# Performance work log

Measured on AMD Instinct MI355X. Metric: run time of the kernel, lower is better.

## Reference

```python
import jax, jax.numpy as jnp
import numpy as np

FEAT = 256
BS = 64
L = 2048
TAU = 2.0          # maxTemp * tempDecay**0 with numUpdates=0
MIN_SEG = 3.0      # minSegmentWidth
NEG_BIG = -10000.0


def setup_inputs() -> dict:
    key = jax.random.key(0)
    ks = jax.random.split(key, 8)
    s = 1.0 / np.sqrt(FEAT)  # PyTorch LSTM/Linear uniform init bound
    x = jax.random.normal(ks[0], (BS, L, FEAT), jnp.float32)
    label = jax.random.randint(ks[1], (BS, L), 0, 2)
    # LSTM cell params (PyTorch layout: gates ordered i, f, g, o)
    W_ih = jax.random.uniform(ks[2], (4 * FEAT, FEAT + 1), jnp.float32, -s, s)
    W_hh = jax.random.uniform(ks[3], (4 * FEAT, FEAT), jnp.float32, -s, s)
    b_ih = jax.random.uniform(ks[4], (4 * FEAT,), jnp.float32, -s, s)
    b_hh = jax.random.uniform(ks[5], (4 * FEAT,), jnp.float32, -s, s)
    # policy: Linear(featuresDim, 2)
    Wp = jax.random.uniform(ks[6], (2, FEAT), jnp.float32, -s, s)
    bp = jax.random.uniform(ks[7], (2,), jnp.float32, -s, s)
    return {"x": x, "label": label, "W_ih": W_ih, "W_hh": W_hh,
            "b_ih": b_ih, "b_hh": b_hh, "Wp": Wp, "bp": bp}


def reference(x, label, W_ih, W_hh, b_ih, b_hh, Wp, bp):
    # label is accepted by the original forward but never used.
    bs, l, d = x.shape

    def step(carry, xt):
        prev_b, flag, h, c = carry  # prev boundary [bs], noBoundaryFlag [bs], LSTM state [bs,d]
        inp = jnp.concatenate([prev_b[:, None], xt], axis=-1)  # [bs, d+1]
        gates = inp @ W_ih.T + h @ W_hh.T + b_ih + b_hh        # [bs, 4d]
        i, f, g, o = jnp.split(gates, 4, axis=-1)
        c = jax.nn.sigmoid(f) * c + jax.nn.sigmoid(i) * jnp.tanh(g)
        h = jax.nn.sigmoid(o) * jnp.tanh(c)
        logits = h @ Wp.T + bp                                 # [bs, 2]
        # mask boundary logit where a boundary was emitted within minSegmentWidth
        logits = logits.at[:, 1].add(jnp.where(flag > 0, NEG_BIG, 0.0))
        logp = jax.nn.log_softmax(logits / TAU, axis=-1)
        samp = jnp.argmax(logp, axis=-1)                       # eval-mode sampling
        flag = jnp.where(flag > 0, flag - 1.0, flag)
        flag = jnp.where(samp > 0, MIN_SEG, flag)
        return (samp.astype(x.dtype), flag, h, c), (logp, samp)

    init = (jnp.zeros((bs,), x.dtype), jnp.zeros((bs,), x.dtype),
            jnp.zeros((bs, d), x.dtype), jnp.zeros((bs, d), x.dtype))
    _, (logps, samps) = jax.lax.scan(step, init, jnp.swapaxes(x, 0, 1))
    logps = jnp.swapaxes(logps, 0, 1)                  # [bs, l, 2]
    boundaries = jnp.swapaxes(samps, 0, 1).astype(x.dtype)  # [bs, l]
    sel = jnp.take_along_axis(logps, boundaries[..., None].astype(jnp.int32), axis=-1)  # [bs, l, 1]
    return boundaries, sel
```

## Files before the change

kernel.cpp:

```cpp
#include <hip/hip_runtime.h>
#include <cstdint>
#include <cmath>

#define FEAT 256
#define GATES 1024
#define BS 64
#define SEQ 2048
#define NEG_BIG -10000.0f
#define MIN_SEG 3.0f

#define KK_REG 24
#define KK_LDS 8
#define KK_STA (KK_REG + KK_LDS)
#define NGEMM 192

#define M0_WPB  262144
#define M0_BIAS 263168
#define M0_H    264192
#define M0_C    280576
#define M0_PF   296960
#define M0_XP   297984
#define M1_WIT  262144
#define M1_WPB  524288
#define M1_BIAS 525312

template<int MODE>
__global__ __launch_bounds__(1024) void prep_kernel(
    const float* __restrict__ W_ih, const float* __restrict__ W_hh,
    const float* __restrict__ b_ih, const float* __restrict__ b_hh,
    float* __restrict__ ws)
{
    const int k = blockIdx.x;
    const int j = threadIdx.x;
    ws[k * GATES + j] = W_hh[(size_t)j * FEAT + k];
    if (MODE == 1)
        ws[M1_WIT + k * GATES + j] = W_ih[(size_t)j * (FEAT + 1) + 1 + k];
    if (k == 0) {
        const int WPB = MODE ? M1_WPB : M0_WPB;
        const int BIA = MODE ? M1_BIAS : M0_BIAS;
        ws[WPB + j] = W_ih[(size_t)j * (FEAT + 1)];
        ws[BIA + j] = b_ih[j] + b_hh[j];
    }
    if (MODE == 0 && k == 1) {
#pragma unroll
        for (int i = 0; i < 16; ++i) {
            ws[M0_H + i * 1024 + j] = 0.f;
            ws[M0_C + i * 1024 + j] = 0.f;
        }
        if (j < 128) ws[M0_PF + j] = 0.f;
    }
}

__global__ __launch_bounds__(256) void xproj_gemm(
    const float* __restrict__ x, const float* __restrict__ W_ih,
    float* __restrict__ ws, int t0, int xpoff)
{
    const int trow = blockIdx.y;
    const int t  = t0 + trow;
    const int j0 = blockIdx.x * 64;
    const int tid = threadIdx.x;
    const int ty = tid >> 4, tx = tid & 15;
    const float* bias = ws + M0_BIAS;
    float* XP = ws + xpoff;
    __shared__ __align__(16) float As[64][65];
    __shared__ __align__(16) float Bs[64][65];
    float acc[4][4] = {};
    for (int k0 = 0; k0 < FEAT; k0 += 64) {
#pragma unroll
        for (int i = 0; i < 16; ++i) {
            int idx = i * 256 + tid;
            int rr = idx >> 6, cc = idx & 63;
            As[rr][cc] = x[((size_t)rr * SEQ + t) * FEAT + k0 + cc];
        }
#pragma unroll
        for (int i = 0; i < 16; ++i) {
            int idx = i * 256 + tid;
            int jj = idx >> 6, kk = idx & 63;
            Bs[kk][jj] = W_ih[(size_t)(j0 + jj) * (FEAT + 1) + 1 + k0 + kk];
        }
        __syncthreads();
#pragma unroll
        for (int kk = 0; kk < 64; ++kk) {
            float a[4], bv[4];
#pragma unroll
            for (int r = 0; r < 4; ++r) a[r] = As[ty * 4 + r][kk];
#pragma unroll
            for (int c = 0; c < 4; ++c) bv[c] = Bs[kk][tx * 4 + c];
#pragma unroll
            for (int r = 0; r < 4; ++r)
#pragma unroll
                for (int c = 0; c < 4; ++c)
                    acc[r][c] = fmaf(a[r], bv[c], acc[r][c]);
        }
        __syncthreads();
    }
#pragma unroll
    for (int r = 0; r < 4; ++r) {
        int bb = ty * 4 + r;
        size_t base = ((size_t)trow * BS + bb) * GATES + j0 + tx * 4;
        float4 v;
        v.x = acc[r][0] + bias[j0 + tx * 4 + 0];
        v.y = acc[r][1] + bias[j0 + tx * 4 + 1];
        v.z = acc[r][2] + bias[j0 + tx * 4 + 2];
        v.w = acc[r][3] + bias[j0 + tx * 4 + 3];
        *(float4*)&XP[base] = v;
    }
}

#define FMA4(acc, hb, wv) \
    acc.x = fmaf(hb, wv.x, acc.x); acc.y = fmaf(hb, wv.y, acc.y); \
    acc.z = fmaf(hb, wv.z, acc.z); acc.w = fmaf(hb, wv.w, acc.w);

__global__ __launch_bounds__(1024, 1) void fused_kernel(
    const float* __restrict__ x, const float* __restrict__ W_ih,
    float* __restrict__ ws,
    const float* __restrict__ Wp, const float* __restrict__ bp,
    float* __restrict__ out_b, float* __restrict__ out_sel,
    int t0, int Tlen, int xp_cur, int xp_nxt)
{
    __shared__ __align__(16) float smem[39178];
    const int tid = threadIdx.x;

    if (blockIdx.x >= BS) {
        if (xp_nxt < 0) return;
        float* As = smem;
        float* Bs = smem + 4160;
        const float* bias = ws + M0_BIAS;
        float* XPn = ws + xp_nxt;
        const int ty = tid >> 6, tx = tid & 63;
        const int jobs = Tlen * 4;
        for (int job = blockIdx.x - BS; job < jobs; job += NGEMM) {
            const int trow = job >> 2;
            const int j0 = (job & 3) * 256;
            const int t = t0 + Tlen + trow;
            float acc[4][4] = {};
            for (int k0 = 0; k0 < FEAT; k0 += 64) {
                __syncthreads();
#pragma unroll
                for (int i = 0; i < 4; ++i) {
                    int idx = i * 1024 + tid, rr = idx >> 6, cc = idx & 63;
                    As[rr * 65 + cc] = x[((size_t)rr * SEQ + t) * FEAT + k0 + cc];
                }
#pragma unroll
                for (int i = 0; i < 16; ++i) {
                    int idx = i * 1024 + tid, jj = idx >> 6, kk = idx & 63;
                    Bs[kk * 260 + jj] = W_ih[(size_t)(j0 + jj) * (FEAT + 1) + 1 + k0 + kk];
                }
                __syncthreads();
#pragma unroll
                for (int kk = 0; kk < 64; ++kk) {
                    float4 bv = *(const float4*)&Bs[kk * 260 + tx * 4];
                    float a[4];
#pragma unroll
                    for (int r = 0; r < 4; ++r) a[r] = As[(ty * 4 + r) * 65 + kk];
#pragma unroll
                    for (int r = 0; r < 4; ++r) {
                        acc[r][0] = fmaf(a[r], bv.x, acc[r][0]);
                        acc[r][1] = fmaf(a[r], bv.y, acc[r][1]);
                        acc[r][2] = fmaf(a[r], bv.z, acc[r][2]);
                        acc[r][3] = fmaf(a[r], bv.w, acc[r][3]);
                    }
                }
            }
#pragma unroll
            for (int r = 0; r < 4; ++r) {
                int bb = ty * 4 + r;
                size_t base = ((size_t)trow * BS + bb) * GATES + j0 + tx * 4;
                float4 v;
                v.x = acc[r][0] + bias[j0 + tx * 4 + 0];
                v.y = acc[r][1] + bias[j0 + tx * 4 + 1];
                v.z = acc[r][2] + bias[j0 + tx * 4 + 2];
                v.w = acc[r][3] + bias[j0 + tx * 4 + 3];
                *(float4*)&XPn[base] = v;
            }
        }
        return;
    }

    const int b   = blockIdx.x;
    const int ch  = tid >> 8;
    const int j4  = (tid & 255) * 4;
    const int f   = tid & 255;
    const int kbase = ch * 64;

    const float* WT   = ws;
    const float* WPB  = ws + M0_WPB;
    float* H  = ws + M0_H;
    float* C  = ws + M0_C;
    float* PF = ws + M0_PF;
    const float* XPc = ws + xp_cur;

    float* wlds   = smem;
    float* part   = smem + 32768;
    float* h_lds  = smem + 36864;
    float* xp_lds = smem + 37120;
    float* red    = smem + 39168;
    float* s_pv   = smem + 39176;

    float4 wreg[KK_REG];
#pragma unroll
    for (int kk = 0; kk < KK_REG; ++kk)
        wreg[kk] = *(const float4*)&WT[(size_t)(kbase + kk) * GATES + j4];
#pragma unroll
    for (int i = 0; i < 4 * KK_LDS; ++i) {
        int ch2 = i / KK_LDS, kkl = i % KK_LDS;
        wlds[i * 1024 + tid] = WT[(size_t)(ch2 * 64 + KK_REG + kkl) * GATES + tid];
    }

    float wpbr[4] = {};
    float wp0 = 0.f, wp1 = 0.f, c_reg = 0.f;
    if (tid < FEAT) {
#pragma unroll
        for (int g = 0; g < 4; ++g) wpbr[g] = WPB[g * FEAT + f];
        wp0 = Wp[f]; wp1 = Wp[FEAT + f];
        c_reg = C[b * FEAT + f];
        h_lds[f] = H[b * FEAT + f];
    }
    const float bp0 = bp[0], bp1 = bp[1];
    xp_lds[tid] = XPc[(size_t)b * GATES + tid];
    if (tid == 0) { s_pv[0] = PF[b * 2 + 0]; s_pv[1] = PF[b * 2 + 1]; }
    __syncthreads();

    float fl_r = 0.f;
    if (tid == 0) fl_r = s_pv[1];

    for (int tl = 0; tl < Tlen; ++tl) {
        const int t   = t0 + tl;
        const int buf = tl & 1;

        float xpf = 0.f;
        const bool haspf = (tl + 1 < Tlen);
        if (haspf) xpf = XPc[((size_t)(tl + 1) * BS + b) * GATES + tid];

        float4 acc = make_float4(0.f, 0.f, 0.f, 0.f);
#pragma unroll
        for (int kk = 0; kk < KK_REG; ++kk) {
            float hb = h_lds[kbase + kk];
            FMA4(acc, hb, wreg[kk]);
        }
#pragma unroll
        for (int kk = 0; kk < KK_LDS; ++kk) {
            float hb = h_lds[kbase + KK_REG + kk];
            float4 wv = *(const float4*)&wlds[(ch * KK_LDS + kk) * 1024 + j4];
            FMA4(acc, hb, wv);
        }
#pragma unroll 4
        for (int kk = KK_STA; kk < 64; ++kk) {
            float hb = h_lds[kbase + kk];
            float4 wv = *(const float4*)&WT[(size_t)(kbase + kk) * GATES + j4];
            FMA4(acc, hb, wv);
        }
        *(float4*)&part[ch * 1024 + j4] = acc;
        __syncthreads();

        if (haspf) xp_lds[(buf ^ 1) * 1024 + tid] = xpf;

        if (tid < FEAT) {
            const float pvv = s_pv[0];
            float gv[4];
#pragma unroll
            for (int g = 0; g < 4; ++g) {
                const int jj = g * FEAT + f;
                gv[g] = part[jj] + part[1024 + jj] + part[2048 + jj] + part[3072 + jj]
                      + xp_lds[buf * 1024 + jj] + pvv * wpbr[g];
            }
            float ig = 1.f / (1.f + expf(-gv[0]));
            float fg = 1.f / (1.f + expf(-gv[1]));
            float gt = tanhf(gv[2]);
            float og = 1.f / (1.f + expf(-gv[3]));
            c_reg = fg * c_reg + ig * gt;
            float h = og * tanhf(c_reg);
            h_lds[f] = h;
            if (tl == Tlen - 1) {
                H[b * FEAT + f] = h;
                C[b * FEAT + f] = c_reg;
            }
            float p0 = h * wp0, p1 = h * wp1;
#pragma unroll
            for (int off = 32; off > 0; off >>= 1) {
                p0 += __shfl_xor(p0, off, 64);
                p1 += __shfl_xor(p1, off, 64);
            }
            if ((tid & 63) == 0) {
                red[tid >> 6] = p0;
                red[4 + (tid >> 6)] = p1;
            }
        }
        __syncthreads();

        if (tid == 0) {
            float l0 = red[0] + red[1] + red[2] + red[3] + bp0;
            float l1 = red[4] + red[5] + red[6] + red[7] + bp1;
            if (fl_r > 0.0f) l1 += NEG_BIG;
            int samp = (l1 > l0) ? 1 : 0;
            float a0 = l0 * 0.5f, a1 = l1 * 0.5f;
            float m = fmaxf(a0, a1);
            float lse = m + logf(expf(a0 - m) + expf(a1 - m));
            out_b[(size_t)b * SEQ + t]   = (float)samp;
            out_sel[(size_t)b * SEQ + t] = (samp ? a1 : a0) - lse;
            fl_r = (fl_r > 0.0f) ? (fl_r - 1.0f) : fl_r;
            if (samp) fl_r = MIN_SEG;
            s_pv[0] = (float)samp;
            if (tl == Tlen - 1) {
                PF[b * 2 + 0] = (float)samp;
                PF[b * 2 + 1] = fl_r;
            }
        }
    }
}

__global__ __launch_bounds__(1024) void consumer1(
    const float* __restrict__ x, float* __restrict__ ws,
    const float* __restrict__ Wp, const float* __restrict__ bp,
    float* __restrict__ out_b, float* __restrict__ out_sel)
{
    const int b   = blockIdx.x;
    const int tid = threadIdx.x;
    const int ch  = tid >> 8;
    const int j4  = (tid & 255) * 4;
    const int f   = tid & 255;
    const int kbase = ch * 64;

    const float* WT   = ws;
    const float* WIT  = ws + M1_WIT;
    const float* WPB  = ws + M1_WPB;
    const float* BIAS = ws + M1_BIAS;

    __shared__ __align__(16) float part[4][GATES];
    __shared__ __align__(16) float h_lds[FEAT];
    __shared__ __align__(16) float x_lds[2][FEAT];
    __shared__ float red[8];
    __shared__ float s_pv[2];

    float biasr[4] = {}, wpbr[4] = {};
    float wp0 = 0.f, wp1 = 0.f, c_reg = 0.f;
    if (tid < FEAT) {
#pragma unroll
        for (int g = 0; g < 4; ++g) {
            wpbr[g]  = WPB[g * FEAT + f];
            biasr[g] = BIAS[g * FEAT + f];
        }
        wp0 = Wp[f]; wp1 = Wp[FEAT + f];
        h_lds[f] = 0.f;
        x_lds[0][f] = x[(size_t)b * SEQ * FEAT + f];
    }
    const float bp0 = bp[0], bp1 = bp[1];
    if (tid == 0) { s_pv[0] = 0.f; s_pv[1] = 0.f; }
    __syncthreads();

    float fl_r = 0.f;
    for (int t = 0; t < SEQ; ++t) {
        const int buf = t & 1;
        float xpf = 0.f;
        const bool haspf = (t + 1 < SEQ) && (tid < FEAT);
        if (haspf) xpf = x[((size_t)b * SEQ + (t + 1)) * FEAT + f];

        float4 acc = make_float4(0.f, 0.f, 0.f, 0.f);
#pragma unroll 4
        for (int kk = 0; kk < 64; ++kk) {
            float hb = h_lds[kbase + kk];
            float4 wv = *(const float4*)&WT[(size_t)(kbase + kk) * GATES + j4];
            FMA4(acc, hb, wv);
            float xb = x_lds[buf][kbase + kk];
            float4 wi = *(const float4*)&WIT[(size_t)(kbase + kk) * GATES + j4];
            FMA4(acc, xb, wi);
        }
        *(float4*)&part[ch][j4] = acc;
        __syncthreads();
        if (haspf) x_lds[buf ^ 1][f] = xpf;

        if (tid < FEAT) {
            const float pvv = s_pv[0];
            float gv[4];
#pragma unroll
            for (int g = 0; g < 4; ++g) {
                const int jj = g * FEAT + f;
                gv[g] = part[0][jj] + part[1][jj] + part[2][jj] + part[3][jj]
                      + biasr[g] + pvv * wpbr[g];
            }
            float ig = 1.f / (1.f + expf(-gv[0]));
            float fg = 1.f / (1.f + expf(-gv[1]));
            float gt = tanhf(gv[2]);
            float og = 1.f / (1.f + expf(-gv[3]));
            c_reg = fg * c_reg + ig * gt;
            float h = og * tanhf(c_reg);
            h_lds[f] = h;
            float p0 = h * wp0, p1 = h * wp1;
#pragma unroll
            for (int off = 32; off > 0; off >>= 1) {
                p0 += __shfl_xor(p0, off, 64);
                p1 += __shfl_xor(p1, off, 64);
            }
            if ((tid & 63) == 0) { red[tid >> 6] = p0; red[4 + (tid >> 6)] = p1; }
        }
        __syncthreads();

        if (tid == 0) {
            float l0 = red[0] + red[1] + red[2] + red[3] + bp0;
            float l1 = red[4] + red[5] + red[6] + red[7] + bp1;
            if (fl_r > 0.0f) l1 += NEG_BIG;
            int samp = (l1 > l0) ? 1 : 0;
            float a0 = l0 * 0.5f, a1 = l1 * 0.5f;
            float m = fmaxf(a0, a1);
            float lse = m + logf(expf(a0 - m) + expf(a1 - m));
            out_b[(size_t)b * SEQ + t]   = (float)samp;
            out_sel[(size_t)b * SEQ + t] = (samp ? a1 : a0) - lse;
            fl_r = (fl_r > 0.0f) ? (fl_r - 1.0f) : fl_r;
            if (samp) fl_r = MIN_SEG;
            s_pv[0] = (float)samp;
        }
    }
}

extern "C" void kernel_launch(void* const* d_in, const int* in_sizes, int n_in,
                              void* d_out, int out_size, void* d_ws, size_t ws_size,
                              hipStream_t stream)
{
    const float* x    = (const float*)d_in[0];
    const float* W_ih = (const float*)d_in[2];
    const float* W_hh = (const float*)d_in[3];
    const float* b_ih = (const float*)d_in[4];
    const float* b_hh = (const float*)d_in[5];
    const float* Wp   = (const float*)d_in[6];
    const float* bp   = (const float*)d_in[7];

    float* ws      = (float*)d_ws;
    float* out_b   = (float*)d_out;
    float* out_sel = out_b + (size_t)BS * SEQ;

    int T = 0;
    for (int cand = 128; cand >= 8; cand >>= 1) {
        size_t need = ((size_t)M0_XP + 2 * (size_t)cand * BS * GATES) * sizeof(float);
        if (ws_size >= need) { T = cand; break; }
    }

    if (T > 0) {
        hipLaunchKernelGGL((prep_kernel<0>), dim3(FEAT), dim3(GATES), 0, stream,
                           W_ih, W_hh, b_ih, b_hh, ws);
        const int win_f = T * BS * GATES;
        const int nch = SEQ / T;
        hipLaunchKernelGGL(xproj_gemm, dim3(GATES / 64, T), dim3(256), 0, stream,
                           x, W_ih, ws, 0, M0_XP);
        for (int c = 0; c < nch; ++c) {
            const int xp_cur = M0_XP + (c & 1) * win_f;
            const int xp_nxt = (c + 1 < nch) ? (M0_XP + ((c + 1) & 1) * win_f) : -1;
            hipLaunchKernelGGL(fused_kernel, dim3(BS + NGEMM), dim3(1024), 0, stream,
                               x, W_ih, ws, Wp, bp, out_b, out_sel,
                               c * T, T, xp_cur, xp_nxt);
        }
    } else {
        hipLaunchKernelGGL((prep_kernel<1>), dim3(FEAT), dim3(GATES), 0, stream,
                           W_ih, W_hh, b_ih, b_hh, ws);
        hipLaunchKernelGGL(consumer1, dim3(BS), dim3(1024), 0, stream,
                           x, ws, Wp, bp, out_b, out_sel);
    }
}
```

Baseline: 13.85 ms.

## Halve block size to 512 threads and split recurrence K into two chunks

The fused recurrent kernel now runs 512 threads per block. Each thread covers 128 of the hidden dimension instead of 64, keeping 40 weight rows in registers and 16 in LDS, so only two partial sums are reduced per gate instead of four. The side GEMM blocks now compute 8 rows per thread to match the smaller block. The intent is to keep more of W_hh on chip per thread and cut reduction and sync work per step. The cost is much higher register pressure, with a risk of spills, and fewer threads to hide latency.

```diff
diff --git a/kernel.cpp b/kernel.cpp
--- a/kernel.cpp
+++ b/kernel.cpp
@@ -9,9 +9,10 @@
 #define NEG_BIG -10000.0f
 #define MIN_SEG 3.0f
 
-#define KK_REG 24
-#define KK_LDS 8
+#define KK_REG 40
+#define KK_LDS 16
 #define KK_STA (KK_REG + KK_LDS)
+#define KPC 128
 #define NGEMM 192
 
 #define M0_WPB  262144
@@ -23,6 +24,14 @@
 #define M1_WIT  262144
 #define M1_WPB  524288
 #define M1_BIAS 525312
+
+#define S_WLDS 0
+#define S_PART 32768
+#define S_XP   34816
+#define S_H    36864
+#define S_RED  37120
+#define S_PV   37128
+#define S_TOT  37130
 
 template<int MODE>
 __global__ __launch_bounds__(1024) void prep_kernel(
@@ -111,14 +120,14 @@
     acc.x = fmaf(hb, wv.x, acc.x); acc.y = fmaf(hb, wv.y, acc.y); \
     acc.z = fmaf(hb, wv.z, acc.z); acc.w = fmaf(hb, wv.w, acc.w);
 
-__global__ __launch_bounds__(1024, 1) void fused_kernel(
+__global__ __launch_bounds__(512, 1) void fused_kernel(
     const float* __restrict__ x, const float* __restrict__ W_ih,
     float* __restrict__ ws,
     const float* __restrict__ Wp, const float* __restrict__ bp,
     float* __restrict__ out_b, float* __restrict__ out_sel,
     int t0, int Tlen, int xp_cur, int xp_nxt)
 {
-    __shared__ __align__(16) float smem[39178];
+    __shared__ __align__(16) float smem[S_TOT];
     const int tid = threadIdx.x;
 
     if (blockIdx.x >= BS) {
@@ -127,44 +136,42 @@
         float* Bs = smem + 4160;
         const float* bias = ws + M0_BIAS;
         float* XPn = ws + xp_nxt;
-        const int ty = tid >> 6, tx = tid & 63;
+        const int tx = tid & 63, ty = tid >> 6;
         const int jobs = Tlen * 4;
         for (int job = blockIdx.x - BS; job < jobs; job += NGEMM) {
             const int trow = job >> 2;
             const int j0 = (job & 3) * 256;
             const int t = t0 + Tlen + trow;
-            float acc[4][4] = {};
+            float acc[8][4] = {};
             for (int k0 = 0; k0 < FEAT; k0 += 64) {
                 __syncthreads();
 #pragma unroll
-                for (int i = 0; i < 4; ++i) {
-                    int idx = i * 1024 + tid, rr = idx >> 6, cc = idx & 63;
+                for (int i = 0; i < 8; ++i) {
+                    int idx = i * 512 + tid, rr = idx >> 6, cc = idx & 63;
                     As[rr * 65 + cc] = x[((size_t)rr * SEQ + t) * FEAT + k0 + cc];
                 }
 #pragma unroll
-                for (int i = 0; i < 16; ++i) {
-                    int idx = i * 1024 + tid, jj = idx >> 6, kk = idx & 63;
+                for (int i = 0; i < 32; ++i) {
+                    int idx = i * 512 + tid, jj = idx >> 6, kk = idx & 63;
                     Bs[kk * 260 + jj] = W_ih[(size_t)(j0 + jj) * (FEAT + 1) + 1 + k0 + kk];
                 }
                 __syncthreads();
-#pragma unroll
+#pragma unroll 4
                 for (int kk = 0; kk < 64; ++kk) {
                     float4 bv = *(const float4*)&Bs[kk * 260 + tx * 4];
-                    float a[4];
-#pragma unroll
-                    for (int r = 0; r < 4; ++r) a[r] = As[(ty * 4 + r) * 65 + kk];
-#pragma unroll
-                    for (int r = 0; r < 4; ++r) {
-                        acc[r][0] = fmaf(a[r], bv.x, acc[r][0]);
-                        acc[r][1] = fmaf(a[r], bv.y, acc[r][1]);
-                        acc[r][2] = fmaf(a[r], bv.z, acc[r][2]);
-                        acc[r][3] = fmaf(a[r], bv.w, acc[r][3]);
+#pragma unroll
+                    for (int r = 0; r < 8; ++r) {
+                        float a = As[(ty * 8 + r) * 65 + kk];
+                        acc[r][0] = fmaf(a, bv.x, acc[r][0]);
+                        acc[r][1] = fmaf(a, bv.y, acc[r][1]);
+                        acc[r][2] = fmaf(a, bv.z, acc[r][2]);
+                        acc[r][3] = fmaf(a, bv.w, acc[r][3]);
                     }
                 }
             }
 #pragma unroll
-            for (int r = 0; r < 4; ++r) {
-                int bb = ty * 4 + r;
+            for (int r = 0; r < 8; ++r) {
+                int bb = ty * 8 + r;
                 size_t base = ((size_t)trow * BS + bb) * GATES + j0 + tx * 4;
                 float4 v;
                 v.x = acc[r][0] + bias[j0 + tx * 4 + 0];
@@ -181,30 +188,32 @@
     const int ch  = tid >> 8;
     const int j4  = (tid & 255) * 4;
     const int f   = tid & 255;
-    const int kbase = ch * 64;
-
-    const float* WT   = ws;
-    const float* WPB  = ws + M0_WPB;
+    const int kbase = ch * KPC;
+
+    const float* WT  = ws;
+    const float* WPB = ws + M0_WPB;
     float* H  = ws + M0_H;
     float* C  = ws + M0_C;
     float* PF = ws + M0_PF;
     const float* XPc = ws + xp_cur;
 
-    float* wlds   = smem;
-    float* part   = smem + 32768;
-    float* h_lds  = smem + 36864;
-    float* xp_lds = smem + 37120;
-    float* red    = smem + 39168;
-    float* s_pv   = smem + 39176;
+    float* wlds   = smem + S_WLDS;
+    float* part   = smem + S_PART;
+    float* xp_lds = smem + S_XP;
+    float* h_lds  = smem + S_H;
+    float* red    = smem + S_RED;
+    float* s_pv   = smem + S_PV;
 
     float4 wreg[KK_REG];
 #pragma unroll
     for (int kk = 0; kk < KK_REG; ++kk)
         wreg[kk] = *(const float4*)&WT[(size_t)(kbase + kk) * GATES + j4];
 #pragma unroll
-    for (int i = 0; i < 4 * KK_LDS; ++i) {
-        int ch2 = i / KK_LDS, kkl = i % KK_LDS;
-        wlds[i * 1024 + tid] = WT[(size_t)(ch2 * 64 + KK_REG + kkl) * GATES + tid];
+    for (int i = 0; i < 64; ++i) {
+        int idx = i * 512 + tid;
+        int row = idx >> 10, col = idx & 1023;
+        int ch2 = row >> 4, kkl = row & 15;
+        wlds[row * 1024 + col] = WT[(size_t)(ch2 * KPC + KK_REG + kkl) * GATES + col];
     }
 
     float wpbr[4] = {};
@@ -217,7 +226,8 @@
         h_lds[f] = H[b * FEAT + f];
     }
     const float bp0 = bp[0], bp1 = bp[1];
-    xp_lds[tid] = XPc[(size_t)b * GATES + tid];
+    xp_lds[tid]       = XPc[(size_t)b * GATES + tid];
+    xp_lds[tid + 512] = XPc[(size_t)b * GATES + tid + 512];
     if (tid == 0) { s_pv[0] = PF[b * 2 + 0]; s_pv[1] = PF[b * 2 + 1]; }
     __syncthreads();
 
@@ -228,9 +238,12 @@
         const int t   = t0 + tl;
         const int buf = tl & 1;
 
-        float xpf = 0.f;
+        float xpf0 = 0.f, xpf1 = 0.f;
         const bool haspf = (tl + 1 < Tlen);
-        if (haspf) xpf = XPc[((size_t)(tl + 1) * BS + b) * GATES + tid];
+        if (haspf) {
+            const float* xr = XPc + ((size_t)(tl + 1) * BS + b) * GATES;
+            xpf0 = xr[tid]; xpf1 = xr[tid + 512];
+        }
 
         float4 acc = make_float4(0.f, 0.f, 0.f, 0.f);
 #pragma unroll
@@ -244,8 +257,8 @@
             float4 wv = *(const float4*)&wlds[(ch * KK_LDS + kk) * 1024 + j4];
             FMA4(acc, hb, wv);
         }
-#pragma unroll 4
-        for (int kk = KK_STA; kk < 64; ++kk) {
+#pragma unroll 8
+        for (int kk = KK_STA; kk < KPC; ++kk) {
             float hb = h_lds[kbase + kk];
             float4 wv = *(const float4*)&WT[(size_t)(kbase + kk) * GATES + j4];
             FMA4(acc, hb, wv);
@@ -253,7 +266,10 @@
         *(float4*)&part[ch * 1024 + j4] = acc;
         __syncthreads();
 
-        if (haspf) xp_lds[(buf ^ 1) * 1024 + tid] = xpf;
+        if (haspf) {
+            xp_lds[(buf ^ 1) * 1024 + tid]       = xpf0;
+            xp_lds[(buf ^ 1) * 1024 + tid + 512] = xpf1;
+        }
 
         if (tid < FEAT) {
             const float pvv = s_pv[0];
@@ -261,7 +277,7 @@
 #pragma unroll
             for (int g = 0; g < 4; ++g) {
                 const int jj = g * FEAT + f;
-                gv[g] = part[jj] + part[1024 + jj] + part[2048 + jj] + part[3072 + jj]
+                gv[g] = part[jj] + part[1024 + jj]
                       + xp_lds[buf * 1024 + jj] + pvv * wpbr[g];
             }
             float ig = 1.f / (1.f + expf(-gv[0]));
@@ -444,7 +460,7 @@
         for (int c = 0; c < nch; ++c) {
             const int xp_cur = M0_XP + (c & 1) * win_f;
             const int xp_nxt = (c + 1 < nch) ? (M0_XP + ((c + 1) & 1) * win_f) : -1;
-            hipLaunchKernelGGL(fused_kernel, dim3(BS + NGEMM), dim3(1024), 0, stream,
+            hipLaunchKernelGGL(fused_kernel, dim3(BS + NGEMM), dim3(512), 0, stream,
                                x, W_ih, ws, Wp, bp, out_b, out_sel,
                                c * T, T, xp_cur, xp_nxt);
         }
```

Measured after the change: 11.41 ms. -17.6%, faster.
